# Kernel optimization log

Measured on AMD Instinct MI355X. Metric: run time of the kernel, lower is better.

## Reference

```python
import jax, jax.numpy as jnp
import numpy as np

N_NODES = 100000
N_EDGES = 1600000
IN_DIM = 128
HIDDEN = 128


def setup_inputs() -> dict:
    key = jax.random.key(0)
    k1, k2, k3, k4 = jax.random.split(key, 4)
    x = jax.random.normal(k1, (N_NODES, IN_DIM), dtype=jnp.float32)
    edge_index = jax.random.randint(k2, (2, N_EDGES), 0, N_NODES, dtype=jnp.int32)
    # Glorot-ish scale (module zero-inits weights, which would give trivial
    # outputs; use random weights for a meaningful correctness baseline).
    W1 = jax.random.normal(k3, (IN_DIM, HIDDEN), dtype=jnp.float32) * (1.0 / np.sqrt(IN_DIM))
    W2 = jax.random.normal(k4, (HIDDEN, HIDDEN), dtype=jnp.float32) * (1.0 / np.sqrt(HIDDEN))
    return {"x": x, "edge_index": edge_index, "W1": W1, "W2": W2}


def _gcn_conv(h, W, src, dst, norm):
    # linear transform then normalized scatter-add aggregation (PyG GCNConv, bias=False)
    h = h @ W                              # [N, H]
    msg = h[src] * norm[:, None]           # gather + scale: [E+N, H]
    return jax.ops.segment_sum(msg, dst, num_segments=N_NODES)


def reference(x, edge_index, W1, W2):
    # add self-loops
    loops = jnp.arange(N_NODES, dtype=edge_index.dtype)
    src = jnp.concatenate([edge_index[0], loops])
    dst = jnp.concatenate([edge_index[1], loops])
    # symmetric normalization D^{-1/2} (A+I) D^{-1/2}; deg >= 1 due to self-loops
    deg = jax.ops.segment_sum(jnp.ones_like(dst, dtype=x.dtype), dst, num_segments=N_NODES)
    dinv = jax.lax.rsqrt(deg)
    norm = dinv[src] * dinv[dst]           # [E+N]

    h = _gcn_conv(x, W1, src, dst, norm)
    h = jax.nn.relu(h)                     # dropout is identity in eval mode
    h = _gcn_conv(h, W2, src, dst, norm)
    return h
```

## Files before the change

kernel.cpp:

```cpp
#include <hip/hip_runtime.h>
#include <hip/hip_bf16.h>

typedef unsigned short u16;
typedef unsigned int   u32;

typedef __attribute__((ext_vector_type(8))) short short8;
typedef __attribute__((ext_vector_type(4))) float floatx4;

#define HD __device__ __forceinline__

HD float bf16_lo(u32 u) { union { u32 i; float f; } v; v.i = u << 16; return v.f; }
HD float bf16_hi(u32 u) { union { u32 i; float f; } v; v.i = u & 0xffff0000u; return v.f; }
HD u16 f2bf(float f) {
    __hip_bfloat16 h = __float2bfloat16(f);
    u16 s; __builtin_memcpy(&s, &h, 2); return s;
}

#define NPB   256
#define MAXNB 512
#define CH    4096
#define CAP   5120

__global__ void k_wprep(const u32* __restrict__ xw,
                        const void* __restrict__ W1, const void* __restrict__ W2,
                        u16* __restrict__ W1t, u16* __restrict__ W2t,
                        int* __restrict__ flag, int* __restrict__ gbcursor) {
    __shared__ int cnt;
    if (threadIdx.x == 0) cnt = 0;
    __syncthreads();
    int sane = 0;
    for (int i = threadIdx.x; i < 4096; i += 256) {
        u32 v = xw[i];
        int e = (v >> 7) & 0xFF;
        sane += (e >= 107 && e <= 147) ? 1 : 0;
    }
    atomicAdd(&cnt, sane);
    __syncthreads();
    int isbf = (cnt > 2048) ? 1 : 0;
    if (blockIdx.x == 0) {
        if (threadIdx.x == 0) *flag = isbf;
        for (int i = threadIdx.x; i <= MAXNB; i += 256) gbcursor[i] = i * CAP;
    }
    int i = blockIdx.x * blockDim.x + threadIdx.x;
    int w = i >> 14;
    int r = (i >> 7) & 127;
    int c = i & 127;
    const void* W = w ? W2 : W1;
    u16*       Wt = w ? W2t : W1t;
    u16 val;
    if (isbf) val = ((const u16*)W)[c * 128 + r];
    else      val = f2bf(((const float*)W)[c * 128 + r]);
    Wt[r * 128 + c] = val;
}

template <int MODE>
__device__ __forceinline__
void gemm_body(u16* __restrict__ lw, u16* __restrict__ st_all,
               const void* __restrict__ inp, const u16* __restrict__ Wt,
               u16* __restrict__ outb, int ntiles, int isbf, int gw, int nw) {
    int lane = threadIdx.x & 63;
    int wid  = threadIdx.x >> 6;
    int m = lane & 15, q = lane >> 4;
    u16* st = st_all + wid * (16 * 136);

    {
        int r = threadIdx.x >> 1;
        int h = threadIdx.x & 1;
        const short8* src = (const short8*)(Wt + r * 128 + h * 64);
#pragma unroll
        for (int jj = 0; jj < 8; jj++) {
            int slot = h * 8 + jj;
            *(short8*)&lw[r * 128 + ((slot ^ (r & 7)) << 3)] = src[jj];
        }
    }
    __syncthreads();

    for (int t = gw; t < ntiles; t += nw) {
        long r0 = (long)t * 32;
        floatx4 acc[2][8];
#pragma unroll
        for (int g = 0; g < 2; g++)
#pragma unroll
            for (int nt = 0; nt < 8; nt++) acc[g][nt] = (floatx4)0.0f;

        short8 a[2][4];
        if (MODE == 1 || isbf) {
#pragma unroll
            for (int g = 0; g < 2; g++)
#pragma unroll
                for (int kk = 0; kk < 4; kk++)
                    a[g][kk] = *(const short8*)((const u16*)inp +
                                 (r0 + g * 16 + m) * 128 + kk * 32 + q * 8);
        } else {
#pragma unroll
            for (int g = 0; g < 2; g++)
#pragma unroll
                for (int kk = 0; kk < 4; kk++) {
                    const float4* fp = (const float4*)((const float*)inp +
                                 (r0 + g * 16 + m) * 128 + kk * 32 + q * 8);
                    float4 f0 = fp[0], f1 = fp[1];
                    short8 v;
                    v[0] = (short)f2bf(f0.x); v[1] = (short)f2bf(f0.y);
                    v[2] = (short)f2bf(f0.z); v[3] = (short)f2bf(f0.w);
                    v[4] = (short)f2bf(f1.x); v[5] = (short)f2bf(f1.y);
                    v[6] = (short)f2bf(f1.z); v[7] = (short)f2bf(f1.w);
                    a[g][kk] = v;
                }
        }

#pragma unroll
        for (int kk = 0; kk < 4; kk++) {
#pragma unroll
            for (int nt = 0; nt < 8; nt++) {
                int slot = kk * 4 + q;
                short8 b = *(const short8*)&lw[(nt * 16 + m) * 128 +
                                               ((slot ^ (m & 7)) << 3)];
                acc[0][nt] = __builtin_amdgcn_mfma_f32_16x16x32_bf16(a[0][kk], b, acc[0][nt], 0, 0, 0);
                acc[1][nt] = __builtin_amdgcn_mfma_f32_16x16x32_bf16(a[1][kk], b, acc[1][nt], 0, 0, 0);
            }
        }

#pragma unroll
        for (int g = 0; g < 2; g++) {
#pragma unroll
            for (int nt = 0; nt < 8; nt++)
#pragma unroll
                for (int i = 0; i < 4; i++)
                    st[(q * 4 + i) * 136 + nt * 16 + m] = f2bf(acc[g][nt][i]);
            __builtin_amdgcn_s_waitcnt(0);
            u16* gbase = outb + (size_t)(r0 + g * 16) * 128;
#pragma unroll
            for (int j = 0; j < 4; j++) {
                int e   = lane * 8 + j * 512;
                int row = e >> 7, colu = e & 127;
                short8 vv = *(const short8*)&st[row * 136 + colu];
                *(short8*)(gbase + e) = vv;
            }
            __builtin_amdgcn_s_waitcnt(0);
        }
    }
}

__device__ __forceinline__
void coarse_body(char* smem, const int* __restrict__ ei, int* __restrict__ gbcursor,
                 int2* __restrict__ pairs, int E, int chunk) {
    int*  hist = (int*)smem;
    int*  gs   = hist + MAXNB;
    int*  dlt  = gs + MAXNB;
    int*  lofs = dlt + MAXNB;
    int2* lp   = (int2*)(smem + 8192);
    u16*  pb   = (u16*)(smem + 8192 + CH * 8);
    const int* srcp = ei;
    const int* dstp = ei + E;
    int base = chunk * CH;
    int cnt  = min(CH, E - base);

    for (int i = threadIdx.x; i < MAXNB; i += 256) hist[i] = 0;
    __syncthreads();

    int2 e[16];
    int nb_ = 0;
#pragma unroll
    for (int j = 0; j < 16; j++) {
        int i = base + threadIdx.x + j * 256;
        if (i < E) {
            e[j].x = srcp[i];
            e[j].y = dstp[i];
            atomicAdd(&hist[e[j].y >> 8], 1);
            nb_ = j + 1;
        }
    }
    __syncthreads();

    if (threadIdx.x < 64) {
        int lane = threadIdx.x;
        int carry = 0;
#pragma unroll
        for (int t = 0; t < MAXNB / 64; t++) {
            int i = t * 64 + lane;
            int v = hist[i];
            int x = v;
#pragma unroll
            for (int off = 1; off < 64; off <<= 1) {
                int y = __shfl_up(x, off);
                if (lane >= off) x += y;
            }
            gs[i] = carry + x - v;
            carry += __shfl(x, 63);
        }
    }
    __syncthreads();

    for (int b = threadIdx.x; b < MAXNB; b += 256) {
        int c = hist[b];
        lofs[b] = gs[b];
        if (c > 0) {
            int gbase = atomicAdd(&gbcursor[b], c);
            dlt[b] = gbase - gs[b];
        }
    }
    __syncthreads();

    for (int j = 0; j < nb_; j++) {
        int b = e[j].y >> 8;
        int p = atomicAdd(&lofs[b], 1);
        lp[p] = e[j];
        pb[p] = (u16)b;
    }
    __syncthreads();

    for (int p = threadIdx.x; p < cnt; p += 256) {
        pairs[p + dlt[pb[p]]] = lp[p];
    }
}

__global__ void __launch_bounds__(256)
k_fused1(const void* __restrict__ x, const u16* __restrict__ W1t,
         u16* __restrict__ Hb, int ntiles, const int* __restrict__ flagp,
         const int* __restrict__ ei, int* __restrict__ gbcursor,
         int2* __restrict__ pairs, int E, int gemmBlocks) {
    __shared__ __align__(16) char smem[50176];
    if (blockIdx.x < gemmBlocks) {
        int isbf = *flagp;
        int gw = (blockIdx.x * 256 + threadIdx.x) >> 6;
        int nw = gemmBlocks * 4;
        gemm_body<0>((u16*)smem, (u16*)(smem + 32768), x, W1t, Hb, ntiles, isbf, gw, nw);
    } else {
        coarse_body(smem, ei, gbcursor, pairs, E, blockIdx.x - gemmBlocks);
    }
}

__global__ void __launch_bounds__(256)
k_gemm2(const void* __restrict__ inp, const u16* __restrict__ Wt,
        u16* __restrict__ outb, int ntiles) {
    __shared__ u16 lw[128 * 128];
    __shared__ u16 stage[4][16 * 136];
    int gw = (blockIdx.x * 256 + threadIdx.x) >> 6;
    int nw = (gridDim.x * 256) >> 6;
    gemm_body<1>(lw, &stage[0][0], inp, Wt, outb, ntiles, 1, gw, nw);
}

__global__ void __launch_bounds__(512)
k_bucket(const int2* __restrict__ pairs, const int* __restrict__ gbcursor,
         float* __restrict__ dinv, int* __restrict__ rbeg, int* __restrict__ rend,
         int* __restrict__ col, int N) {
    __shared__ int lc[NPB];
    __shared__ int lcur[NPB];
    __shared__ int ws[4];
    __shared__ int wsoff[4];
    int b = blockIdx.x;
    int nbase = b * NPB;
    int tid = threadIdx.x, lane = tid & 63, wid = tid >> 6;
    if (tid < NPB) lc[tid] = 0;
    __syncthreads();
    int p0 = b * CAP, p1 = gbcursor[b];
    for (int p = p0 + tid; p < p1; p += 512)
        atomicAdd(&lc[pairs[p].y - nbase], 1);
    __syncthreads();
    int v = 0, x = 0, node = nbase + tid;
    if (tid < NPB) {
        v = lc[tid];
        if (node < N) dinv[node] = rsqrtf((float)v + 1.0f);
        x = v;
#pragma unroll
        for (int off = 1; off < 64; off <<= 1) {
            int y = __shfl_up(x, off);
            if (lane >= off) x += y;
        }
        if (lane == 63) ws[wid] = x;
    }
    __syncthreads();
    if (tid == 0) {
        int s = 0;
#pragma unroll
        for (int k2 = 0; k2 < 4; k2++) { wsoff[k2] = s; s += ws[k2]; }
    }
    __syncthreads();
    if (tid < NPB) {
        int excl = p0 + wsoff[wid] + (x - v);
        if (node < N) { rbeg[node] = excl; rend[node] = excl + v; }
        lcur[tid] = excl;
    }
    __syncthreads();
    for (int p = p0 + tid; p < p1; p += 512) {
        int2 e = pairs[p];
        int pos = atomicAdd(&lcur[e.y - nbase], 1);
        col[pos] = e.x;
    }
}

HD void agg_node(const u16* __restrict__ hbl, const int* __restrict__ col,
                 const float* __restrict__ dinv, int r0, int r1, int n,
                 float di, int lane, float& a0o, float& a1o) {
    u32 h = *(const u32*)(hbl + (size_t)n * 128);
    float a0 = bf16_lo(h) * di, a1 = bf16_hi(h) * di;
    for (int base = r0; base < r1; base += 64) {
        int cnt = min(64, r1 - base);
        int   myc = (lane < cnt) ? col[base + lane] : 0;
        float mdv = (lane < cnt) ? dinv[myc] : 0.0f;
        int e = 0;
        for (; e + 15 < cnt; e += 16) {
            u32 hh[16]; float cf[16];
#pragma unroll
            for (int j = 0; j < 16; j++) {
                int s = __builtin_amdgcn_readlane(myc, e + j);
                cf[j] = __int_as_float(__builtin_amdgcn_readlane(__float_as_int(mdv), e + j));
                hh[j] = *(const u32*)(hbl + (size_t)s * 128);
            }
#pragma unroll
            for (int j = 0; j < 16; j++) {
                a0 += bf16_lo(hh[j]) * cf[j];
                a1 += bf16_hi(hh[j]) * cf[j];
            }
        }
        for (; e + 7 < cnt; e += 8) {
            u32 hh[8]; float cf[8];
#pragma unroll
            for (int j = 0; j < 8; j++) {
                int s = __builtin_amdgcn_readlane(myc, e + j);
                cf[j] = __int_as_float(__builtin_amdgcn_readlane(__float_as_int(mdv), e + j));
                hh[j] = *(const u32*)(hbl + (size_t)s * 128);
            }
#pragma unroll
            for (int j = 0; j < 8; j++) {
                a0 += bf16_lo(hh[j]) * cf[j];
                a1 += bf16_hi(hh[j]) * cf[j];
            }
        }
        for (; e + 3 < cnt; e += 4) {
            u32 hh[4]; float cf[4];
#pragma unroll
            for (int j = 0; j < 4; j++) {
                int s = __builtin_amdgcn_readlane(myc, e + j);
                cf[j] = __int_as_float(__builtin_amdgcn_readlane(__float_as_int(mdv), e + j));
                hh[j] = *(const u32*)(hbl + (size_t)s * 128);
            }
#pragma unroll
            for (int j = 0; j < 4; j++) {
                a0 += bf16_lo(hh[j]) * cf[j];
                a1 += bf16_hi(hh[j]) * cf[j];
            }
        }
        for (; e < cnt; e++) {
            int   s  = __builtin_amdgcn_readlane(myc, e);
            float cf = __int_as_float(__builtin_amdgcn_readlane(__float_as_int(mdv), e));
            u32  hh  = *(const u32*)(hbl + (size_t)s * 128);
            a0 += bf16_lo(hh) * cf; a1 += bf16_hi(hh) * cf;
        }
    }
    a0o = a0 * di; a1o = a1 * di;
}

template <int MODE>
__global__ void k_csr_agg(const u16* __restrict__ Hb, const int* __restrict__ col,
                          const int* __restrict__ rbeg, const int* __restrict__ rend,
                          const float* __restrict__ dinv,
                          void* __restrict__ outp, int N, const int* __restrict__ flagp) {
    int isbf = MODE ? *flagp : 1;
    int gw   = (blockIdx.x * blockDim.x + threadIdx.x) >> 6;
    int nw   = (gridDim.x * blockDim.x) >> 6;
    int lane = threadIdx.x & 63;
    const u16* hbl = Hb + lane * 2;
    for (int n = gw; n < N; n += nw) {
        float a0, a1;
        agg_node(hbl, col, dinv, rbeg[n], rend[n], n, dinv[n], lane, a0, a1);
        if (MODE == 0) {
            float r0f = fmaxf(a0, 0.0f), r1f = fmaxf(a1, 0.0f);
            ((u32*)outp)[(size_t)n * 64 + lane] = (u32)f2bf(r0f) | ((u32)f2bf(r1f) << 16);
        } else if (isbf) {
            ((u32*)outp)[(size_t)n * 64 + lane] = (u32)f2bf(a0) | ((u32)f2bf(a1) << 16);
        } else {
            ((float2*)outp)[(size_t)n * 64 + lane] = make_float2(a0, a1);
        }
    }
}

extern "C" void kernel_launch(void* const* d_in, const int* in_sizes, int n_in,
                              void* d_out, int out_size, void* d_ws, size_t ws_size,
                              hipStream_t stream) {
    const void* x  = d_in[0];
    const int*  ei = (const int*)d_in[1];
    const void* W1 = d_in[2];
    const void* W2 = d_in[3];

    const int N = in_sizes[0] / 128;
    const int E = in_sizes[1] / 2;

    char* ws = (char*)d_ws;
    float* dinv    = (float*)ws;
    int*   rbeg    = (int*)(ws + (512u << 10));
    int*   rend    = (int*)(ws + (1024u << 10));
    int*   gbcur   = (int*)(ws + (1536u << 10));
    int*   flag    = (int*)(ws + (1600u << 10));
    u16*   W1t     = (u16*)(ws + (2048u << 10));
    u16*   W2t     = W1t + 128 * 128;
    int*   col     = (int*)(ws + (3u << 20));
    u16*   Hb      = (u16*)(ws + (12u << 20));
    u16*   A       = (u16*)(ws + (38u << 20));
    int2*  pairs   = (int2*)(ws + (64u << 20));

    int NB  = (N + NPB - 1) / NPB;
    int nch = (E + CH - 1) / CH;

    int ntiles     = N / 32;
    int gemmBlocks = (ntiles + 3) / 4;
    int ablocks    = (N + 3) / 4;

    k_wprep<<<128, 256, 0, stream>>>((const u32*)x, W1, W2, W1t, W2t, flag, gbcur);
    k_fused1<<<gemmBlocks + nch, 256, 0, stream>>>(x, W1t, Hb, ntiles, flag,
                                                   ei, gbcur, pairs, E, gemmBlocks);
    k_bucket<<<NB, 512, 0, stream>>>(pairs, gbcur, dinv, rbeg, rend, col, N);

    k_csr_agg<0><<<ablocks, 256, 0, stream>>>(Hb, col, rbeg, rend, dinv, A, N, flag);

    k_gemm2<<<gemmBlocks, 256, 0, stream>>>(A, W2t, Hb, ntiles);
    k_csr_agg<1><<<ablocks, 256, 0, stream>>>(Hb, col, rbeg, rend, dinv, d_out, N, flag);
}
```

Baseline: 308.8 us.

## Hold GEMM B fragments in registers, stage A in LDS, shrink edge chunks

```diff
diff --git a/kernel.cpp b/kernel.cpp
--- a/kernel.cpp
+++ b/kernel.cpp
@@ -18,7 +18,7 @@
 
 #define NPB   256
 #define MAXNB 512
-#define CH    4096
+#define CH    2048
 #define CAP   5120
 
 __global__ void k_wprep(const u32* __restrict__ xw,
@@ -55,88 +55,81 @@
 
 template <int MODE>
 __device__ __forceinline__
-void gemm_body(u16* __restrict__ lw, u16* __restrict__ st_all,
+void gemm_regB(u16* __restrict__ stA, u16* __restrict__ stC,
                const void* __restrict__ inp, const u16* __restrict__ Wt,
-               u16* __restrict__ outb, int ntiles, int isbf, int gw, int nw) {
-    int lane = threadIdx.x & 63;
-    int wid  = threadIdx.x >> 6;
+               u16* __restrict__ outb, int ntiles, int isbf, int blk, int nblk) {
+    int tid  = threadIdx.x;
+    int lane = tid & 63, wid = tid >> 6;
     int m = lane & 15, q = lane >> 4;
-    u16* st = st_all + wid * (16 * 136);
-
-    {
-        int r = threadIdx.x >> 1;
-        int h = threadIdx.x & 1;
-        const short8* src = (const short8*)(Wt + r * 128 + h * 64);
-#pragma unroll
-        for (int jj = 0; jj < 8; jj++) {
-            int slot = h * 8 + jj;
-            *(short8*)&lw[r * 128 + ((slot ^ (r & 7)) << 3)] = src[jj];
-        }
-    }
-    __syncthreads();
-
-    for (int t = gw; t < ntiles; t += nw) {
+
+    short8 bfr[2][4];
+#pragma unroll
+    for (int ntl = 0; ntl < 2; ntl++)
+#pragma unroll
+        for (int kk = 0; kk < 4; kk++)
+            bfr[ntl][kk] = *(const short8*)(Wt + ((wid * 2 + ntl) * 16 + m) * 128 +
+                                            kk * 32 + q * 8);
+
+    int arow = tid >> 3;
+    int achk = tid & 7;
+
+    for (int t = blk; t < ntiles; t += nblk) {
         long r0 = (long)t * 32;
-        floatx4 acc[2][8];
+        if (MODE == 1 || isbf) {
+            const u16* src = (const u16*)inp + (r0 + arow) * 128 + achk * 16;
+            *(short8*)&stA[arow * 136 + achk * 16]     = *(const short8*)(src);
+            *(short8*)&stA[arow * 136 + achk * 16 + 8] = *(const short8*)(src + 8);
+        } else {
+            const float4* fp = (const float4*)((const float*)inp +
+                               (r0 + arow) * 128 + achk * 16);
+            float4 f0 = fp[0], f1 = fp[1], f2 = fp[2], f3 = fp[3];
+            short8 v0, v1;
+            v0[0] = (short)f2bf(f0.x); v0[1] = (short)f2bf(f0.y);
+            v0[2] = (short)f2bf(f0.z); v0[3] = (short)f2bf(f0.w);
+            v0[4] = (short)f2bf(f1.x); v0[5] = (short)f2bf(f1.y);
+            v0[6] = (short)f2bf(f1.z); v0[7] = (short)f2bf(f1.w);
+            v1[0] = (short)f2bf(f2.x); v1[1] = (short)f2bf(f2.y);
+            v1[2] = (short)f2bf(f2.z); v1[3] = (short)f2bf(f2.w);
+            v1[4] = (short)f2bf(f3.x); v1[5] = (short)f2bf(f3.y);
+            v1[6] = (short)f2bf(f3.z); v1[7] = (short)f2bf(f3.w);
+            *(short8*)&stA[arow * 136 + achk * 16]     = v0;
+            *(short8*)&stA[arow * 136 + achk * 16 + 8] = v1;
+        }
+        __syncthreads();
+
+        floatx4 acc[2][2];
 #pragma unroll
         for (int g = 0; g < 2; g++)
 #pragma unroll
-            for (int nt = 0; nt < 8; nt++) acc[g][nt] = (floatx4)0.0f;
-
-        short8 a[2][4];
-        if (MODE == 1 || isbf) {
-#pragma unroll
-            for (int g = 0; g < 2; g++)
-#pragma unroll
-                for (int kk = 0; kk < 4; kk++)
-                    a[g][kk] = *(const short8*)((const u16*)inp +
-                                 (r0 + g * 16 + m) * 128 + kk * 32 + q * 8);
-        } else {
-#pragma unroll
-            for (int g = 0; g < 2; g++)
-#pragma unroll
-                for (int kk = 0; kk < 4; kk++) {
-                    const float4* fp = (const float4*)((const float*)inp +
-                                 (r0 + g * 16 + m) * 128 + kk * 32 + q * 8);
-                    float4 f0 = fp[0], f1 = fp[1];
-                    short8 v;
-                    v[0] = (short)f2bf(f0.x); v[1] = (short)f2bf(f0.y);
-                    v[2] = (short)f2bf(f0.z); v[3] = (short)f2bf(f0.w);
-                    v[4] = (short)f2bf(f1.x); v[5] = (short)f2bf(f1.y);
-                    v[6] = (short)f2bf(f1.z); v[7] = (short)f2bf(f1.w);
-                    a[g][kk] = v;
-                }
-        }
+            for (int ntl = 0; ntl < 2; ntl++) acc[g][ntl] = (floatx4)0.0f;
 
 #pragma unroll
         for (int kk = 0; kk < 4; kk++) {
-#pragma unroll
-            for (int nt = 0; nt < 8; nt++) {
-                int slot = kk * 4 + q;
-                short8 b = *(const short8*)&lw[(nt * 16 + m) * 128 +
-                                               ((slot ^ (m & 7)) << 3)];
-                acc[0][nt] = __builtin_amdgcn_mfma_f32_16x16x32_bf16(a[0][kk], b, acc[0][nt], 0, 0, 0);
-                acc[1][nt] = __builtin_amdgcn_mfma_f32_16x16x32_bf16(a[1][kk], b, acc[1][nt], 0, 0, 0);
-            }
-        }
-
-#pragma unroll
-        for (int g = 0; g < 2; g++) {
-#pragma unroll
-            for (int nt = 0; nt < 8; nt++)
+            short8 a0 = *(const short8*)&stA[m * 136 + kk * 32 + q * 8];
+            short8 a1 = *(const short8*)&stA[(16 + m) * 136 + kk * 32 + q * 8];
+            acc[0][0] = __builtin_amdgcn_mfma_f32_16x16x32_bf16(a0, bfr[0][kk], acc[0][0], 0, 0, 0);
+            acc[0][1] = __builtin_amdgcn_mfma_f32_16x16x32_bf16(a0, bfr[1][kk], acc[0][1], 0, 0, 0);
+            acc[1][0] = __builtin_amdgcn_mfma_f32_16x16x32_bf16(a1, bfr[0][kk], acc[1][0], 0, 0, 0);
+            acc[1][1] = __builtin_amdgcn_mfma_f32_16x16x32_bf16(a1, bfr[1][kk], acc[1][1], 0, 0, 0);
+        }
+
+#pragma unroll
+        for (int g = 0; g < 2; g++)
+#pragma unroll
+            for (int ntl = 0; ntl < 2; ntl++)
 #pragma unroll
                 for (int i = 0; i < 4; i++)
-                    st[(q * 4 + i) * 136 + nt * 16 + m] = f2bf(acc[g][nt][i]);
-            __builtin_amdgcn_s_waitcnt(0);
-            u16* gbase = outb + (size_t)(r0 + g * 16) * 128;
-#pragma unroll
-            for (int j = 0; j < 4; j++) {
-                int e   = lane * 8 + j * 512;
-                int row = e >> 7, colu = e & 127;
-                short8 vv = *(const short8*)&st[row * 136 + colu];
-                *(short8*)(gbase + e) = vv;
-            }
-            __builtin_amdgcn_s_waitcnt(0);
+                    stC[(g * 16 + q * 4 + i) * 136 + (wid * 2 + ntl) * 16 + m] =
+                        f2bf(acc[g][ntl][i]);
+        __syncthreads();
+
+        u16* gbase = outb + (size_t)r0 * 128;
+#pragma unroll
+        for (int j = 0; j < 2; j++) {
+            int e   = tid * 8 + j * 2048;
+            int row = e >> 7, colu = e & 127;
+            short8 vv = *(const short8*)&stC[row * 136 + colu];
+            *(short8*)(gbase + e) = vv;
         }
     }
 }
@@ -149,7 +142,6 @@
     int*  dlt  = gs + MAXNB;
     int*  lofs = dlt + MAXNB;
     int2* lp   = (int2*)(smem + 8192);
-    u16*  pb   = (u16*)(smem + 8192 + CH * 8);
     const int* srcp = ei;
     const int* dstp = ei + E;
     int base = chunk * CH;
@@ -158,10 +150,10 @@
     for (int i = threadIdx.x; i < MAXNB; i += 256) hist[i] = 0;
     __syncthreads();
 
-    int2 e[16];
+    int2 e[CH / 256];
     int nb_ = 0;
 #pragma unroll
-    for (int j = 0; j < 16; j++) {
+    for (int j = 0; j < CH / 256; j++) {
         int i = base + threadIdx.x + j * 256;
         if (i < E) {
             e[j].x = srcp[i];
@@ -205,12 +197,12 @@
         int b = e[j].y >> 8;
         int p = atomicAdd(&lofs[b], 1);
         lp[p] = e[j];
-        pb[p] = (u16)b;
     }
     __syncthreads();
 
     for (int p = threadIdx.x; p < cnt; p += 256) {
-        pairs[p + dlt[pb[p]]] = lp[p];
+        int2 v = lp[p];
+        pairs[p + dlt[v.y >> 8]] = v;
     }
 }
 
@@ -219,12 +211,11 @@
          u16* __restrict__ Hb, int ntiles, const int* __restrict__ flagp,
          const int* __restrict__ ei, int* __restrict__ gbcursor,
          int2* __restrict__ pairs, int E, int gemmBlocks) {
-    __shared__ __align__(16) char smem[50176];
+    __shared__ __align__(16) char smem[24576];
     if (blockIdx.x < gemmBlocks) {
         int isbf = *flagp;
-        int gw = (blockIdx.x * 256 + threadIdx.x) >> 6;
-        int nw = gemmBlocks * 4;
-        gemm_body<0>((u16*)smem, (u16*)(smem + 32768), x, W1t, Hb, ntiles, isbf, gw, nw);
+        gemm_regB<0>((u16*)smem, (u16*)(smem + 8704), x, W1t, Hb, ntiles,
+                     isbf, blockIdx.x, gemmBlocks);
     } else {
         coarse_body(smem, ei, gbcursor, pairs, E, blockIdx.x - gemmBlocks);
     }
@@ -233,11 +224,8 @@
 __global__ void __launch_bounds__(256)
 k_gemm2(const void* __restrict__ inp, const u16* __restrict__ Wt,
         u16* __restrict__ outb, int ntiles) {
-    __shared__ u16 lw[128 * 128];
-    __shared__ u16 stage[4][16 * 136];
-    int gw = (blockIdx.x * 256 + threadIdx.x) >> 6;
-    int nw = (gridDim.x * 256) >> 6;
-    gemm_body<1>(lw, &stage[0][0], inp, Wt, outb, ntiles, 1, gw, nw);
+    __shared__ __align__(16) u16 st[2][32 * 136];
+    gemm_regB<1>(st[0], st[1], inp, Wt, outb, ntiles, 1, blockIdx.x, gridDim.x);
 }
 
 __global__ void __launch_bounds__(512)
@@ -403,7 +391,7 @@
     int nch = (E + CH - 1) / CH;
 
     int ntiles     = N / 32;
-    int gemmBlocks = (ntiles + 3) / 4;
+    int gemmBlocks = 782;
     int ablocks    = (N + 3) / 4;
 
     k_wprep<<<128, 256, 0, stream>>>((const u32*)x, W1, W2, W1t, W2t, flag, gbcur);
```

Result: faster. 301.3 us (-2.4%).
